# Kernel optimization log

Hardware: AMD Instinct MI355X
Metric: run time of the kernel (lower is better)

## Reference

```python
import jax, jax.numpy as jnp
import numpy as np

N_LAYERS = 4
HIDDEN = 64
OUT_DIM = 32
IN_DIM = 32
NUM_GRAPHS = 128
N_NODES = 100000
N_EDGES = 1600000


def setup_inputs() -> dict:
    key = jax.random.key(0)
    ks = jax.random.split(key, 20)
    s = 0.05
    inp = {
        "x_q": jax.random.normal(ks[0], (N_NODES, IN_DIM), jnp.float32),
        "edge_index_q": jax.random.randint(ks[1], (2, N_EDGES), 0, N_NODES),
        "batch_q": jnp.sort(jax.random.randint(ks[2], (N_NODES,), 0, NUM_GRAPHS)),
        "x_c": jax.random.normal(ks[3], (N_NODES, IN_DIM), jnp.float32),
        "edge_index_c": jax.random.randint(ks[4], (2, N_EDGES), 0, N_NODES),
        "batch_c": jnp.sort(jax.random.randint(ks[5], (N_NODES,), 0, NUM_GRAPHS)),
        "pre_w": jax.random.normal(ks[6], (IN_DIM, HIDDEN), jnp.float32) * s,
        "pre_b": jnp.zeros((HIDDEN,), jnp.float32),
        "conv_w1": jax.random.normal(ks[7], (N_LAYERS, HIDDEN, HIDDEN), jnp.float32) * s,
        "conv_b1": jnp.zeros((N_LAYERS, HIDDEN), jnp.float32),
        "conv_w2": jax.random.normal(ks[8], (N_LAYERS, HIDDEN, HIDDEN), jnp.float32) * s,
        "conv_b2": jnp.zeros((N_LAYERS, HIDDEN), jnp.float32),
        "post_w1": jax.random.normal(ks[9], (HIDDEN * (N_LAYERS + 1), HIDDEN), jnp.float32) * s,
        "post_b1": jnp.zeros((HIDDEN,), jnp.float32),
        "post_w2": jax.random.normal(ks[10], (HIDDEN, OUT_DIM), jnp.float32) * s,
        "post_b2": jnp.zeros((OUT_DIM,), jnp.float32),
    }
    return inp


def _embed(x, edge_index, batch, pre_w, pre_b, conv_w1, conv_b1, conv_w2, conv_b2,
           post_w1, post_b1, post_w2, post_b2):
    n = x.shape[0]
    src, dst = edge_index[0], edge_index[1]
    x = x @ pre_w + pre_b                       # [N, H]
    emb = [x]
    xres = x
    for i in range(N_LAYERS):
        # GINConv (eps=0): nn(x + sum_{j in N(i)} x_j)
        agg = jax.ops.segment_sum(x[src], dst, num_segments=n)
        h = x + agg
        h = jax.nn.relu(h @ conv_w1[i] + conv_b1[i]) @ conv_w2[i] + conv_b2[i]
        if i & 1:
            h = h + xres
            xres = h
        x = jax.nn.relu(h)
        emb.append(x)
    e = jnp.concatenate(emb, axis=1)            # [N, H*(L+1)]
    g = jax.ops.segment_sum(e, batch, num_segments=NUM_GRAPHS)  # global_add_pool
    return jax.nn.relu(g @ post_w1 + post_b1) @ post_w2 + post_b2  # [G, OUT]


def reference(x_q, edge_index_q, batch_q, x_c, edge_index_c, batch_c,
              pre_w, pre_b, conv_w1, conv_b1, conv_w2, conv_b2,
              post_w1, post_b1, post_w2, post_b2):
    params = (pre_w, pre_b, conv_w1, conv_b1, conv_w2, conv_b2,
              post_w1, post_b1, post_w2, post_b2)
    gx = _embed(x_q, edge_index_q, batch_q, *params)
    hx = _embed(x_c, edge_index_c, batch_c, *params)
    # asymm_norm with all costs = 1: (del+edge_del)*0.5 = 1.0 each side
    return (jax.nn.relu(gx - hx) * 1.0).sum(-1) + (jax.nn.relu(hx - gx) * 1.0).sum(-1)
```

## Files before the change

kernel.cpp:

```cpp
#include <hip/hip_runtime.h>

#define NNODES 100000
#define NEDGES 1600000
#define NG 128
#define HID 64
#define INDIM 32
#define CAT 320
#define ODIM 32

#define BSH 6
#define NPB 64
#define NB ((NNODES + NPB - 1) / NPB)

#define CBSH 9
#define NCB ((NNODES + 511) / 512)
#define R1CHUNK 4096
#define NR1 ((NEDGES + R1CHUNK - 1) / R1CHUNK)
#define CAP 12288

typedef unsigned short ushort_t;

__device__ __forceinline__ float bcast(float v, int lane) {
    return __uint_as_float(__builtin_amdgcn_readlane(__float_as_uint(v), lane));
}
__device__ __forceinline__ unsigned bcast_u(unsigned v, int lane) {
    return __builtin_amdgcn_readlane(v, lane);
}
__device__ __forceinline__ ushort_t f2bf(float f) {
    unsigned u = __float_as_uint(f);
    return (ushort_t)((u + 0x7FFFu + ((u >> 16) & 1u)) >> 16);
}
__device__ __forceinline__ float bf2f(ushort_t h) {
    return __uint_as_float(((unsigned)h) << 16);
}


__global__ void radix1a_kernel(const int* __restrict__ ei, int* __restrict__ ccounts) {
    __shared__ int h[NCB];
    for (int i = threadIdx.x; i < NCB; i += blockDim.x) h[i] = 0;
    __syncthreads();
    int stride = gridDim.x * blockDim.x;
    for (int e = blockIdx.x * blockDim.x + threadIdx.x; e < NEDGES; e += stride)
        atomicAdd(&h[ei[NEDGES + e] >> CBSH], 1);
    __syncthreads();
    for (int i = threadIdx.x; i < NCB; i += blockDim.x)
        if (h[i]) atomicAdd(&ccounts[i], h[i]);
}

__global__ void cscan_kernel(const int* __restrict__ ccounts, int* __restrict__ cstart,
                             int* __restrict__ ccursor) {
    __shared__ int s[256];
    int t = threadIdx.x;
    int v = (t < NCB) ? ccounts[t] : 0;
    s[t] = v;
    for (int off = 1; off < 256; off <<= 1) {
        __syncthreads();
        int a = (t >= off) ? s[t - off] : 0;
        __syncthreads();
        s[t] += a;
    }
    __syncthreads();
    if (t < NCB) { cstart[t] = s[t] - v; ccursor[t] = s[t] - v; }
    if (t == 0) cstart[NCB] = NEDGES;
}

__global__ void __launch_bounds__(256) radix1b_kernel(
        const int* __restrict__ ei, int* __restrict__ ccursor,
        unsigned* __restrict__ packed0) {
    __shared__ int h[256], lstart[256], lpos[256], gbase[256], sc[256];
    __shared__ unsigned sdata[R1CHUNK];
    int t  = threadIdx.x;
    int e0 = blockIdx.x * R1CHUNK;
    int e1 = min(e0 + R1CHUNK, NEDGES);
    h[t] = 0; lpos[t] = 0;
    __syncthreads();
    for (int e = e0 + t; e < e1; e += blockDim.x)
        atomicAdd(&h[ei[NEDGES + e] >> CBSH], 1);
    __syncthreads();
    int v = h[t];
    sc[t] = v;
    for (int off = 1; off < 256; off <<= 1) {
        __syncthreads();
        int a = (t >= off) ? sc[t - off] : 0;
        __syncthreads();
        sc[t] += a;
    }
    __syncthreads();
    lstart[t] = sc[t] - v;
    if (t < NCB && v) gbase[t] = atomicAdd(&ccursor[t], v);
    __syncthreads();
    for (int e = e0 + t; e < e1; e += blockDim.x) {
        int dst = ei[NEDGES + e];
        int b   = dst >> CBSH;
        int p   = lstart[b] + atomicAdd(&lpos[b], 1);
        sdata[p] = (unsigned)ei[e] | ((unsigned)(dst & 511) << 20);
    }
    __syncthreads();
    int lane = t & 63, wave = t >> 6;
    for (int b = wave; b < NCB; b += 4) {
        int cnt = h[b];
        if (!cnt) continue;
        int gb = gbase[b], ls = lstart[b];
        for (int i = lane; i < cnt; i += 64) packed0[gb + i] = sdata[ls + i];
    }
}

__global__ void __launch_bounds__(256) radix2_kernel(
        const unsigned* __restrict__ packed0, const int* __restrict__ cstart,
        int* __restrict__ start, unsigned* __restrict__ packed) {
    __shared__ int cnt[512], excl[512], lpos[512], sc[256];
    __shared__ unsigned sdata[CAP];
    int b = blockIdx.x;
    int t = threadIdx.x;
    int s0 = cstart[b], s1 = cstart[b + 1];
    int n  = s1 - s0;
    for (int i = t; i < 512; i += 256) { cnt[i] = 0; lpos[i] = 0; }
    __syncthreads();
    for (int i = t; i < n; i += 256)
        atomicAdd(&cnt[(packed0[s0 + i] >> 20) & 511], 1);
    __syncthreads();
    int a  = cnt[2 * t], c2 = cnt[2 * t + 1];
    int ps = a + c2;
    sc[t] = ps;
    for (int off = 1; off < 256; off <<= 1) {
        __syncthreads();
        int x = (t >= off) ? sc[t - off] : 0;
        __syncthreads();
        sc[t] += x;
    }
    __syncthreads();
    int ex = sc[t] - ps;
    excl[2 * t] = ex; excl[2 * t + 1] = ex + a;
    __syncthreads();
    int node0 = b << CBSH;
    for (int j = t; j < 512; j += 256) {
        int node = node0 + j;
        if (node < NNODES) start[node] = s0 + excl[j];
    }
    if (b == 0 && t == 0) start[NNODES] = NEDGES;
    if (n <= CAP) {
        for (int i = t; i < n; i += 256) {
            unsigned u = packed0[s0 + i];
            int ld = (u >> 20) & 511;
            int p  = excl[ld] + atomicAdd(&lpos[ld], 1);
            sdata[p] = (u & 0xFFFFFu) | ((unsigned)(ld & 63) << 20);
        }
        __syncthreads();
        for (int i = t; i < n; i += 256) packed[s0 + i] = sdata[i];
    } else {
        for (int i = t; i < n; i += 256) {
            unsigned u = packed0[s0 + i];
            int ld = (u >> 20) & 511;
            int p  = s0 + excl[ld] + atomicAdd(&lpos[ld], 1);
            packed[p] = (u & 0xFFFFFu) | ((unsigned)(ld & 63) << 20);
        }
    }
}


#define LOADV(vv, kk) { \
    const ushort_t* ap_ = Xb + (((size_t)(bcast_u(u, (kk)) & 0xFFFFFu)) << 6) + lane; \
    asm volatile("global_load_ushort %0, %1, off" : "=v"(vv) : "v"(ap_)); }

#define PROCJ(vv, kk, cnt) { \
    asm volatile("s_waitcnt vmcnt(" #cnt ")" ::: "memory"); \
    __builtin_amdgcn_sched_barrier(0); \
    int ld_ = (int)(bcast_u(u, (kk)) >> 20); \
    if (ld_ != cur) { \
        if (cur >= 0) atomicAdd(&tile[(cur << 6) + lane], acc); \
        acc = 0.f; cur = ld_; \
    } \
    acc += __uint_as_float((vv) << 16); }

#define LOAD8(P, base) \
    LOADV(P##0, (base)+0) LOADV(P##1, (base)+1) LOADV(P##2, (base)+2) LOADV(P##3, (base)+3) \
    LOADV(P##4, (base)+4) LOADV(P##5, (base)+5) LOADV(P##6, (base)+6) LOADV(P##7, (base)+7)

#define PROC8_HI(P, base) \
    PROCJ(P##0,(base)+0,15) PROCJ(P##1,(base)+1,14) PROCJ(P##2,(base)+2,13) PROCJ(P##3,(base)+3,12) \
    PROCJ(P##4,(base)+4,11) PROCJ(P##5,(base)+5,10) PROCJ(P##6,(base)+6,9)  PROCJ(P##7,(base)+7,8)

#define PROC8_LO(P, base) \
    PROCJ(P##0,(base)+0,7) PROCJ(P##1,(base)+1,6) PROCJ(P##2,(base)+2,5) PROCJ(P##3,(base)+3,4) \
    PROCJ(P##4,(base)+4,3) PROCJ(P##5,(base)+5,2) PROCJ(P##6,(base)+6,1) PROCJ(P##7,(base)+7,0)

__global__ void __launch_bounds__(256, 5) fused_kernel(
        const ushort_t* __restrict__ Xb, ushort_t* __restrict__ Xb_out,
        float* __restrict__ XRES, float* __restrict__ G,
        const int* __restrict__ batch,
        const unsigned* __restrict__ packed, const int* __restrict__ start,
        const float* __restrict__ w1, const float* __restrict__ b1,
        const float* __restrict__ w2, const float* __restrict__ b2,
        int do_res, int stage) {
    __shared__ float tile[NPB * HID];
    __shared__ float sw[HID * HID];
    int blk = blockIdx.x;
    for (int i = threadIdx.x; i < NPB * HID; i += blockDim.x) tile[i] = 0.f;
    {
        const float4* w4 = (const float4*)w1;
        float4* s4 = (float4*)sw;
        for (int i = threadIdx.x; i < HID * HID / 4; i += blockDim.x) s4[i] = w4[i];
    }
    __syncthreads();
    int lane   = threadIdx.x & 63;
    int wave   = threadIdx.x >> 6;
    int nw     = blockDim.x >> 6;
    int node0  = blk << BSH;
    int nvalid = min(NPB, NNODES - node0);
    int eb = start[node0];
    int ee = start[node0 + nvalid];
    for (int base = eb + wave * 64; base < ee; base += nw * 64) {
        int nv = min(64, ee - base);
        unsigned u = (base + lane < ee) ? packed[base + lane] : 0u;
        float acc = 0.f;
        int   cur = -1;
        if (nv == 64) {
            unsigned p0,p1,p2,p3,p4,p5,p6,p7, q0,q1,q2,q3,q4,q5,q6,q7;
            LOAD8(p, 0)
            LOAD8(q, 8)
            PROC8_HI(p, 0)
            LOAD8(p, 16)
            PROC8_HI(q, 8)
            LOAD8(q, 24)
            PROC8_HI(p, 16)
            LOAD8(p, 32)
            PROC8_HI(q, 24)
            LOAD8(q, 40)
            PROC8_HI(p, 32)
            LOAD8(p, 48)
            PROC8_HI(q, 40)
            LOAD8(q, 56)
            PROC8_HI(p, 48)
            PROC8_LO(q, 56)
        } else {
            for (int k = 0; k < nv; ++k) {
                unsigned uj = bcast_u(u, k);
                float vv = bf2f(Xb[((size_t)(uj & 0xFFFFFu) << 6) + lane]);
                atomicAdd(&tile[((uj >> 20) << 6) + lane], vv);
            }
        }
        if (cur >= 0) atomicAdd(&tile[(cur << 6) + lane], acc);
    }
    __syncthreads();
    int per = NPB >> 2;
    int n0w = node0 + wave * per;
    int n1w = min(n0w + per, node0 + nvalid);
    if (n0w < n1w) {
        float bb1 = b1[lane];
        for (int node = n0w; node < n1w; ++node) {
            int row = (node - node0) << 6;
            float in   = bf2f(Xb[((size_t)node << 6) + lane]) + tile[row + lane];
            float acc1 = bb1;
#pragma unroll
            for (int k = 0; k < HID; ++k)
                acc1 = fmaf(bcast(in, k), sw[k * HID + lane], acc1);
            tile[row + lane] = fmaxf(acc1, 0.f);
        }
    }
    __syncthreads();
    {
        const float4* w4 = (const float4*)w2;
        float4* s4 = (float4*)sw;
        for (int i = threadIdx.x; i < HID * HID / 4; i += blockDim.x) s4[i] = w4[i];
    }
    __syncthreads();
    if (n0w < n1w) {
        float bb2 = b2[lane];
        float pool = 0.f;
        int   curg = batch[n0w];
        for (int node = n0w; node < n1w; ++node) {
            float acc2 = bb2;
            const float4* trow = (const float4*)&tile[(node - node0) << 6];
#pragma unroll
            for (int k4 = 0; k4 < HID / 4; ++k4) {
                float4 h = trow[k4];
                acc2 = fmaf(h.x, sw[(4 * k4 + 0) * HID + lane], acc2);
                acc2 = fmaf(h.y, sw[(4 * k4 + 1) * HID + lane], acc2);
                acc2 = fmaf(h.z, sw[(4 * k4 + 2) * HID + lane], acc2);
                acc2 = fmaf(h.w, sw[(4 * k4 + 3) * HID + lane], acc2);
            }
            if (do_res) {
                acc2 += XRES[((size_t)node << 6) + lane];
                XRES[((size_t)node << 6) + lane] = acc2;
            }
            float xn = fmaxf(acc2, 0.f);
            Xb_out[((size_t)node << 6) + lane] = f2bf(xn);
            int g = batch[node];
            if (g != curg) {
                atomicAdd(&G[curg * CAT + stage * HID + lane], pool);
                pool = 0.f; curg = g;
            }
            pool += xn;
        }
        atomicAdd(&G[curg * CAT + stage * HID + lane], pool);
    }
}


__global__ void pre_kernel(const float* __restrict__ xin, const int* __restrict__ batch,
                           const float* __restrict__ w, const float* __restrict__ b,
                           ushort_t* __restrict__ Xb, float* __restrict__ XRES,
                           float* __restrict__ G) {
    __shared__ float sw[INDIM * HID];
    for (int i = threadIdx.x; i < INDIM * HID; i += blockDim.x) sw[i] = w[i];
    __syncthreads();
    int lane = threadIdx.x & 63;
    int wid  = blockIdx.x * (blockDim.x >> 6) + (threadIdx.x >> 6);
    int nW   = gridDim.x * (blockDim.x >> 6);
    int chunk = (NNODES + nW - 1) / nW;
    int n0 = wid * chunk, n1 = min(n0 + chunk, NNODES);
    if (n0 >= n1) return;
    float bb   = b[lane];
    float pool = 0.f;
    int   curg = batch[n0];
    for (int node = n0; node < n1; ++node) {
        float in  = (lane < INDIM) ? xin[node * INDIM + lane] : 0.f;
        float acc = bb;
#pragma unroll
        for (int k = 0; k < INDIM; ++k)
            acc = fmaf(bcast(in, k), sw[k * HID + lane], acc);
        Xb[((size_t)node << 6) + lane]   = f2bf(acc);
        XRES[((size_t)node << 6) + lane] = acc;
        int g = batch[node];
        if (g != curg) {
            atomicAdd(&G[curg * CAT + lane], pool);
            pool = 0.f; curg = g;
        }
        pool += acc;
    }
    atomicAdd(&G[curg * CAT + lane], pool);
}

__global__ void post_kernel(const float* __restrict__ GQ, const float* __restrict__ GC,
                            const float* __restrict__ w1, const float* __restrict__ b1,
                            const float* __restrict__ w2, const float* __restrict__ b2,
                            float* __restrict__ out) {
    int g    = blockIdx.x;
    int lane = threadIdx.x;
    __shared__ float h1q[HID], h1c[HID];
    float aq = b1[lane], ac = b1[lane];
    for (int k = 0; k < CAT; ++k) {
        float w = w1[k * HID + lane];
        aq = fmaf(GQ[g * CAT + k], w, aq);
        ac = fmaf(GC[g * CAT + k], w, ac);
    }
    h1q[lane] = fmaxf(aq, 0.f);
    h1c[lane] = fmaxf(ac, 0.f);
    __syncthreads();
    float s = 0.f;
    if (lane < ODIM) {
        float oq = b2[lane], oc = b2[lane];
        for (int k = 0; k < HID; ++k) {
            float w = w2[k * ODIM + lane];
            oq = fmaf(h1q[k], w, oq);
            oc = fmaf(h1c[k], w, oc);
        }
        s = fabsf(oq - oc);
    }
    for (int off = 16; off; off >>= 1) s += __shfl_down(s, off, 64);
    if (lane == 0) out[g] = s;
}

extern "C" void kernel_launch(void* const* d_in, const int* in_sizes, int n_in,
                              void* d_out, int out_size, void* d_ws, size_t ws_size,
                              hipStream_t stream) {
    const float* x_q     = (const float*)d_in[0];
    const int*   ei_q    = (const int*)d_in[1];
    const int*   batch_q = (const int*)d_in[2];
    const float* x_c     = (const float*)d_in[3];
    const int*   ei_c    = (const int*)d_in[4];
    const int*   batch_c = (const int*)d_in[5];
    const float* pre_w   = (const float*)d_in[6];
    const float* pre_b   = (const float*)d_in[7];
    const float* conv_w1 = (const float*)d_in[8];
    const float* conv_b1 = (const float*)d_in[9];
    const float* conv_w2 = (const float*)d_in[10];
    const float* conv_b2 = (const float*)d_in[11];
    const float* post_w1 = (const float*)d_in[12];
    const float* post_b1 = (const float*)d_in[13];
    const float* post_w2 = (const float*)d_in[14];
    const float* post_b2 = (const float*)d_in[15];

    float* ws   = (float*)d_ws;
    float* XRES = ws;
    float* GQ   = XRES + NNODES * HID;
    float* GC   = GQ + NG * CAT;
    int*   ccounts = (int*)(GC + NG * CAT);
    int*   cstart  = ccounts + NCB;
    int*   ccursor = cstart + NCB + 1;
    int*   start   = ccursor + NCB;
    unsigned* packed0 = (unsigned*)(start + NNODES + 1);
    unsigned* packed  = packed0 + NEDGES;
    ushort_t* XbfA = (ushort_t*)(packed + NEDGES);
    ushort_t* XbfB = XbfA + (size_t)NNODES * HID;

    hipMemsetAsync(GQ, 0, 2 * NG * CAT * sizeof(float), stream);

    for (int side = 0; side < 2; ++side) {
        const float* xin   = side ? x_c : x_q;
        const int*   ei    = side ? ei_c : ei_q;
        const int*   batch = side ? batch_c : batch_q;
        float*       G     = side ? GC : GQ;

        hipMemsetAsync(ccounts, 0, NCB * sizeof(int), stream);
        radix1a_kernel<<<256, 256, 0, stream>>>(ei, ccounts);
        cscan_kernel<<<1, 256, 0, stream>>>(ccounts, cstart, ccursor);
        radix1b_kernel<<<NR1, 256, 0, stream>>>(ei, ccursor, packed0);
        radix2_kernel<<<NCB, 256, 0, stream>>>(packed0, cstart, start, packed);

        pre_kernel<<<1024, 256, 0, stream>>>(xin, batch, pre_w, pre_b, XbfA, XRES, G);

        ushort_t* xcur = XbfA;
        ushort_t* xnxt = XbfB;
        for (int l = 0; l < 4; ++l) {
            fused_kernel<<<NB, 256, 0, stream>>>(xcur, xnxt, XRES, G, batch, packed, start,
                                                 conv_w1 + l * HID * HID, conv_b1 + l * HID,
                                                 conv_w2 + l * HID * HID, conv_b2 + l * HID,
                                                 l & 1, l + 1);
            ushort_t* t = xcur; xcur = xnxt; xnxt = t;
        }
    }

    post_kernel<<<NG, 64, 0, stream>>>(GQ, GC, post_w1, post_b1, post_w2, post_b2,
                                       (float*)d_out);
}
```

Measured before the change: 1.254 ms.

## Split fused GIN layer into gather and MLP kernels with paired-edge dword loads

Splits the fused gather+MLP kernel into a gather_kernel that writes fp32 aggregates to a new AGG buffer and a separate mlp_kernel that runs both matmuls per node. The gather now loads 4 bytes per lane, two edges per wavefront instruction with each half-wave covering one edge, and prefetches the next packed index chunk while processing the current one. The split is meant to give the gather higher occupancy by dropping the weight tiles from its shared memory. In exchange it adds a full fp32 round trip of the aggregates through global memory and an extra launch per layer.

```diff
diff --git a/kernel.cpp b/kernel.cpp
--- a/kernel.cpp
+++ b/kernel.cpp
@@ -158,49 +158,46 @@
 }
 
 
-#define LOADV(vv, kk) { \
-    const ushort_t* ap_ = Xb + (((size_t)(bcast_u(u, (kk)) & 0xFFFFFu)) << 6) + lane; \
-    asm volatile("global_load_ushort %0, %1, off" : "=v"(vv) : "v"(ap_)); }
-
-#define PROCJ(vv, kk, cnt) { \
-    asm volatile("s_waitcnt vmcnt(" #cnt ")" ::: "memory"); \
+#define LOADV2(vv, ss) { \
+    unsigned s0_ = bcast_u(u, 2*(ss))   & 0xFFFFFu; \
+    unsigned s1_ = bcast_u(u, 2*(ss)+1) & 0xFFFFFu; \
+    unsigned ssel_ = (lane < 32) ? s0_ : s1_; \
+    const unsigned* ap_ = Xb4 + (((size_t)ssel_) << 5) + (lane & 31); \
+    asm volatile("global_load_dword %0, %1, off" : "=v"(vv) : "v"(ap_)); }
+
+#define PROCJ2(vv, ss, cnt) { \
+    asm volatile("s_waitcnt vmcnt(" #cnt ")" : "+v"(vv) :: "memory"); \
     __builtin_amdgcn_sched_barrier(0); \
-    int ld_ = (int)(bcast_u(u, (kk)) >> 20); \
-    if (ld_ != cur) { \
-        if (cur >= 0) atomicAdd(&tile[(cur << 6) + lane], acc); \
-        acc = 0.f; cur = ld_; \
+    unsigned d0_ = bcast_u(u, 2*(ss))   >> 20; \
+    unsigned d1_ = bcast_u(u, 2*(ss)+1) >> 20; \
+    unsigned ldd_ = (lane < 32) ? d0_ : d1_; \
+    if (ldd_ != curv) { \
+        float* tp_ = &tile[(curv << 6) + ((lane & 31) << 1)]; \
+        atomicAdd(tp_, accx); atomicAdd(tp_ + 1, accy); \
+        accx = 0.f; accy = 0.f; curv = ldd_; \
     } \
-    acc += __uint_as_float((vv) << 16); }
-
-#define LOAD8(P, base) \
-    LOADV(P##0, (base)+0) LOADV(P##1, (base)+1) LOADV(P##2, (base)+2) LOADV(P##3, (base)+3) \
-    LOADV(P##4, (base)+4) LOADV(P##5, (base)+5) LOADV(P##6, (base)+6) LOADV(P##7, (base)+7)
-
-#define PROC8_HI(P, base) \
-    PROCJ(P##0,(base)+0,15) PROCJ(P##1,(base)+1,14) PROCJ(P##2,(base)+2,13) PROCJ(P##3,(base)+3,12) \
-    PROCJ(P##4,(base)+4,11) PROCJ(P##5,(base)+5,10) PROCJ(P##6,(base)+6,9)  PROCJ(P##7,(base)+7,8)
-
-#define PROC8_LO(P, base) \
-    PROCJ(P##0,(base)+0,7) PROCJ(P##1,(base)+1,6) PROCJ(P##2,(base)+2,5) PROCJ(P##3,(base)+3,4) \
-    PROCJ(P##4,(base)+4,3) PROCJ(P##5,(base)+5,2) PROCJ(P##6,(base)+6,1) PROCJ(P##7,(base)+7,0)
-
-__global__ void __launch_bounds__(256, 5) fused_kernel(
-        const ushort_t* __restrict__ Xb, ushort_t* __restrict__ Xb_out,
-        float* __restrict__ XRES, float* __restrict__ G,
-        const int* __restrict__ batch,
-        const unsigned* __restrict__ packed, const int* __restrict__ start,
-        const float* __restrict__ w1, const float* __restrict__ b1,
-        const float* __restrict__ w2, const float* __restrict__ b2,
-        int do_res, int stage) {
-    __shared__ float tile[NPB * HID];
-    __shared__ float sw[HID * HID];
+    accx += __uint_as_float((vv) << 16); \
+    accy += __uint_as_float((vv) & 0xFFFF0000u); }
+
+#define LOAD8_2(P, base) \
+    LOADV2(P##0, (base)+0) LOADV2(P##1, (base)+1) LOADV2(P##2, (base)+2) LOADV2(P##3, (base)+3) \
+    LOADV2(P##4, (base)+4) LOADV2(P##5, (base)+5) LOADV2(P##6, (base)+6) LOADV2(P##7, (base)+7)
+
+#define PROC8_2HI(P, base) \
+    PROCJ2(P##0,(base)+0,15) PROCJ2(P##1,(base)+1,14) PROCJ2(P##2,(base)+2,13) PROCJ2(P##3,(base)+3,12) \
+    PROCJ2(P##4,(base)+4,11) PROCJ2(P##5,(base)+5,10) PROCJ2(P##6,(base)+6,9)  PROCJ2(P##7,(base)+7,8)
+
+#define PROC8_2LO(P, base) \
+    PROCJ2(P##0,(base)+0,7) PROCJ2(P##1,(base)+1,6) PROCJ2(P##2,(base)+2,5) PROCJ2(P##3,(base)+3,4) \
+    PROCJ2(P##4,(base)+4,3) PROCJ2(P##5,(base)+5,2) PROCJ2(P##6,(base)+6,1) PROCJ2(P##7,(base)+7,0)
+
+__global__ void __launch_bounds__(256, 8) gather_kernel(
+        const ushort_t* __restrict__ Xb, const unsigned* __restrict__ packed,
+        const int* __restrict__ start, float* __restrict__ AGG) {
+    __shared__ float tile[(NPB + 1) * HID];
+    const unsigned* Xb4 = (const unsigned*)Xb;
     int blk = blockIdx.x;
-    for (int i = threadIdx.x; i < NPB * HID; i += blockDim.x) tile[i] = 0.f;
-    {
-        const float4* w4 = (const float4*)w1;
-        float4* s4 = (float4*)sw;
-        for (int i = threadIdx.x; i < HID * HID / 4; i += blockDim.x) s4[i] = w4[i];
-    }
+    for (int i = threadIdx.x; i < (NPB + 1) * HID; i += blockDim.x) tile[i] = 0.f;
     __syncthreads();
     int lane   = threadIdx.x & 63;
     int wave   = threadIdx.x >> 6;
@@ -209,91 +206,103 @@
     int nvalid = min(NPB, NNODES - node0);
     int eb = start[node0];
     int ee = start[node0 + nvalid];
-    for (int base = eb + wave * 64; base < ee; base += nw * 64) {
-        int nv = min(64, ee - base);
-        unsigned u = (base + lane < ee) ? packed[base + lane] : 0u;
-        float acc = 0.f;
-        int   cur = -1;
-        if (nv == 64) {
-            unsigned p0,p1,p2,p3,p4,p5,p6,p7, q0,q1,q2,q3,q4,q5,q6,q7;
-            LOAD8(p, 0)
-            LOAD8(q, 8)
-            PROC8_HI(p, 0)
-            LOAD8(p, 16)
-            PROC8_HI(q, 8)
-            LOAD8(q, 24)
-            PROC8_HI(p, 16)
-            LOAD8(p, 32)
-            PROC8_HI(q, 24)
-            LOAD8(q, 40)
-            PROC8_HI(p, 32)
-            LOAD8(p, 48)
-            PROC8_HI(q, 40)
-            LOAD8(q, 56)
-            PROC8_HI(p, 48)
-            PROC8_LO(q, 56)
-        } else {
-            for (int k = 0; k < nv; ++k) {
-                unsigned uj = bcast_u(u, k);
-                float vv = bf2f(Xb[((size_t)(uj & 0xFFFFFu) << 6) + lane]);
-                atomicAdd(&tile[((uj >> 20) << 6) + lane], vv);
+    int base0 = eb + wave * 64;
+    if (base0 < ee) {
+        unsigned u = (base0 + lane < ee) ? packed[base0 + lane] : 0u;
+        unsigned curv = NPB;
+        float accx = 0.f, accy = 0.f;
+        for (int base = base0; base < ee; base += nw * 64) {
+            int nv    = min(64, ee - base);
+            int nbase = base + nw * 64;
+            unsigned u_next = 0u;
+            int have_next = nbase < ee;
+            if (have_next) {
+                const unsigned* dp_ = packed + nbase + lane;
+                asm volatile("global_load_dword %0, %1, off" : "=v"(u_next) : "v"(dp_));
             }
-        }
-        if (cur >= 0) atomicAdd(&tile[(cur << 6) + lane], acc);
-    }
-    __syncthreads();
-    int per = NPB >> 2;
-    int n0w = node0 + wave * per;
-    int n1w = min(n0w + per, node0 + nvalid);
-    if (n0w < n1w) {
-        float bb1 = b1[lane];
-        for (int node = n0w; node < n1w; ++node) {
-            int row = (node - node0) << 6;
-            float in   = bf2f(Xb[((size_t)node << 6) + lane]) + tile[row + lane];
-            float acc1 = bb1;
+            if (nv == 64) {
+                unsigned p0,p1,p2,p3,p4,p5,p6,p7, q0,q1,q2,q3,q4,q5,q6,q7;
+                LOAD8_2(p, 0)
+                LOAD8_2(q, 8)
+                PROC8_2HI(p, 0)
+                LOAD8_2(p, 16)
+                PROC8_2HI(q, 8)
+                LOAD8_2(q, 24)
+                PROC8_2HI(p, 16)
+                PROC8_2LO(q, 24)
+            } else {
+                float* tp_ = &tile[(curv << 6) + ((lane & 31) << 1)];
+                atomicAdd(tp_, accx); atomicAdd(tp_ + 1, accy);
+                accx = 0.f; accy = 0.f; curv = NPB;
+                for (int k = 0; k < nv; ++k) {
+                    unsigned uj = bcast_u(u, k);
+                    float vv = bf2f(Xb[((size_t)(uj & 0xFFFFFu) << 6) + lane]);
+                    atomicAdd(&tile[((uj >> 20) << 6) + lane], vv);
+                }
+            }
+            if (have_next) {
+                asm volatile("s_waitcnt vmcnt(0)" : "+v"(u_next) :: "memory");
+                u = u_next;
+            }
+        }
+        float* tp_ = &tile[(curv << 6) + ((lane & 31) << 1)];
+        atomicAdd(tp_, accx); atomicAdd(tp_ + 1, accy);
+    }
+    __syncthreads();
+    const float4* t4 = (const float4*)tile;
+    float4* a4 = (float4*)(AGG + ((size_t)node0 << 6));
+    for (int i = threadIdx.x; i < nvalid * (HID / 4); i += blockDim.x) a4[i] = t4[i];
+}
+
+
+__global__ void mlp_kernel(const ushort_t* __restrict__ Xin, ushort_t* __restrict__ Xout,
+                           const float* __restrict__ AGG,
+                           float* __restrict__ XRES, float* __restrict__ G,
+                           const int* __restrict__ batch,
+                           const float* __restrict__ w1, const float* __restrict__ b1,
+                           const float* __restrict__ w2, const float* __restrict__ b2,
+                           int do_res, int stage) {
+    __shared__ float sw1[HID * HID];
+    __shared__ float sw2[HID * HID];
+    for (int i = threadIdx.x; i < HID * HID; i += blockDim.x) {
+        sw1[i] = w1[i];
+        sw2[i] = w2[i];
+    }
+    __syncthreads();
+    int lane = threadIdx.x & 63;
+    int wid  = blockIdx.x * (blockDim.x >> 6) + (threadIdx.x >> 6);
+    int nW   = gridDim.x * (blockDim.x >> 6);
+    int chunk = (NNODES + nW - 1) / nW;
+    int n0 = wid * chunk, n1 = min(n0 + chunk, NNODES);
+    if (n0 >= n1) return;
+    float bb1 = b1[lane], bb2 = b2[lane];
+    float pool = 0.f;
+    int   curg = batch[n0];
+    for (int node = n0; node < n1; ++node) {
+        float in   = bf2f(Xin[((size_t)node << 6) + lane]) + AGG[((size_t)node << 6) + lane];
+        float acc1 = bb1;
 #pragma unroll
-            for (int k = 0; k < HID; ++k)
-                acc1 = fmaf(bcast(in, k), sw[k * HID + lane], acc1);
-            tile[row + lane] = fmaxf(acc1, 0.f);
-        }
-    }
-    __syncthreads();
-    {
-        const float4* w4 = (const float4*)w2;
-        float4* s4 = (float4*)sw;
-        for (int i = threadIdx.x; i < HID * HID / 4; i += blockDim.x) s4[i] = w4[i];
-    }
-    __syncthreads();
-    if (n0w < n1w) {
-        float bb2 = b2[lane];
-        float pool = 0.f;
-        int   curg = batch[n0w];
-        for (int node = n0w; node < n1w; ++node) {
-            float acc2 = bb2;
-            const float4* trow = (const float4*)&tile[(node - node0) << 6];
+        for (int k = 0; k < HID; ++k)
+            acc1 = fmaf(bcast(in, k), sw1[k * HID + lane], acc1);
+        float h1   = fmaxf(acc1, 0.f);
+        float acc2 = bb2;
 #pragma unroll
-            for (int k4 = 0; k4 < HID / 4; ++k4) {
-                float4 h = trow[k4];
-                acc2 = fmaf(h.x, sw[(4 * k4 + 0) * HID + lane], acc2);
-                acc2 = fmaf(h.y, sw[(4 * k4 + 1) * HID + lane], acc2);
-                acc2 = fmaf(h.z, sw[(4 * k4 + 2) * HID + lane], acc2);
-                acc2 = fmaf(h.w, sw[(4 * k4 + 3) * HID + lane], acc2);
-            }
-            if (do_res) {
-                acc2 += XRES[((size_t)node << 6) + lane];
-                XRES[((size_t)node << 6) + lane] = acc2;
-            }
-            float xn = fmaxf(acc2, 0.f);
-            Xb_out[((size_t)node << 6) + lane] = f2bf(xn);
-            int g = batch[node];
-            if (g != curg) {
-                atomicAdd(&G[curg * CAT + stage * HID + lane], pool);
-                pool = 0.f; curg = g;
-            }
-            pool += xn;
-        }
-        atomicAdd(&G[curg * CAT + stage * HID + lane], pool);
-    }
+        for (int k = 0; k < HID; ++k)
+            acc2 = fmaf(bcast(h1, k), sw2[k * HID + lane], acc2);
+        if (do_res) {
+            acc2 += XRES[((size_t)node << 6) + lane];
+            XRES[((size_t)node << 6) + lane] = acc2;
+        }
+        float xn = fmaxf(acc2, 0.f);
+        Xout[((size_t)node << 6) + lane] = f2bf(xn);
+        int g = batch[node];
+        if (g != curg) {
+            atomicAdd(&G[curg * CAT + stage * HID + lane], pool);
+            pool = 0.f; curg = g;
+        }
+        pool += xn;
+    }
+    atomicAdd(&G[curg * CAT + stage * HID + lane], pool);
 }
 
 
@@ -383,15 +392,16 @@
 
     float* ws   = (float*)d_ws;
     float* XRES = ws;
-    float* GQ   = XRES + NNODES * HID;
+    float* AGG  = XRES + NNODES * HID;
+    float* GQ   = AGG + NNODES * HID;
     float* GC   = GQ + NG * CAT;
     int*   ccounts = (int*)(GC + NG * CAT);
     int*   cstart  = ccounts + NCB;
     int*   ccursor = cstart + NCB + 1;
     int*   start   = ccursor + NCB;
     unsigned* packed0 = (unsigned*)(start + NNODES + 1);
-    unsigned* packed  = packed0 + NEDGES;
-    ushort_t* XbfA = (ushort_t*)(packed + NEDGES);
+    unsigned* packed  = packed0 + NEDGES + 64;
+    ushort_t* XbfA = (ushort_t*)(packed + NEDGES + 64);
     ushort_t* XbfB = XbfA + (size_t)NNODES * HID;
 
     hipMemsetAsync(GQ, 0, 2 * NG * CAT * sizeof(float), stream);
@@ -413,7 +423,8 @@
         ushort_t* xcur = XbfA;
         ushort_t* xnxt = XbfB;
         for (int l = 0; l < 4; ++l) {
-            fused_kernel<<<NB, 256, 0, stream>>>(xcur, xnxt, XRES, G, batch, packed, start,
+            gather_kernel<<<NB, 256, 0, stream>>>(xcur, packed, start, AGG);
+            mlp_kernel<<<1024, 256, 0, stream>>>(xcur, xnxt, AGG, XRES, G, batch,
                                                  conv_w1 + l * HID * HID, conv_b1 + l * HID,
                                                  conv_w2 + l * HID * HID, conv_b2 + l * HID,
                                                  l & 1, l + 1);
```

Result: slower. 2.104 ms (+67.8%).
